# Kernel tuning notes

Hardware: AMD Instinct MI355X
Metric: run time of the kernel (lower is better)

## Reference

```python
import jax, jax.numpy as jnp
import numpy as np

B, S, D = 32, 1024, 1025  # batch, seq_length(=num_loci), input_dim
QD, KD = 64, 64
INIT_SCALE = 0.03


def _attention(y, Wq, Wk, Wv):
    # y: [B, S, D]
    q = jnp.einsum('bsd,dq->bsq', y, Wq)
    k = jnp.einsum('bsd,dk->bsk', y, Wk)
    v = jnp.einsum('bsd,de->bse', y, Wv)
    scores = jax.nn.softmax(jnp.einsum('bsq,btq->bst', q, k), axis=-1)
    return jnp.einsum('bst,bte->bse', scores, v)


def setup_inputs() -> dict:
    key = jax.random.key(0)
    ks = jax.random.split(key, 13)
    p = lambda k, shape: INIT_SCALE * jax.random.normal(k, shape, dtype=jnp.float32)
    return {
        'x': jax.random.normal(ks[0], (B, S, D), dtype=jnp.float32),
        'Wq1': p(ks[1], (D, QD)), 'Wk1': p(ks[2], (D, KD)), 'Wv1': p(ks[3], (D, D)),
        'Wq2': p(ks[4], (D, QD)), 'Wk2': p(ks[5], (D, KD)), 'Wv2': p(ks[6], (D, D)),
        'Wq3': p(ks[7], (D, QD)), 'Wk3': p(ks[8], (D, KD)), 'Wv3': p(ks[9], (D, D)),
        'random_matrix': p(ks[10], (S, D - 1)),
        'coeffs_attended': p(ks[11], (S, D)),
        'offset': p(ks[12], (1,)),
    }


def reference(x, Wq1, Wk1, Wv1, Wq2, Wk2, Wv2, Wq3, Wk3, Wv3,
              random_matrix, coeffs_attended, offset):
    # y = concat(x[:, :, :S] @ random_matrix, x[:, :, -1:])  -> [B, S, D]
    y = jnp.concatenate(
        [jnp.einsum('bsf,fe->bse', x[:, :, :S], random_matrix), x[:, :, -1:]],
        axis=2)
    a1 = _attention(y, Wq1, Wk1, Wv1)
    a2 = _attention(a1, Wq2, Wk2, Wv2)
    a3 = _attention(a2, Wq3, Wk3, Wv3)
    out = jnp.einsum('bij,ij->b', a3, coeffs_attended) + offset
    return out
```

## Files before the change

### kernel.cpp

```cpp
#include <hip/hip_runtime.h>
#include <hip/hip_bf16.h>
#include <stdint.h>

typedef __bf16 bf16;
typedef __bf16 bf16x8 __attribute__((ext_vector_type(8)));
typedef float f32x4 __attribute__((ext_vector_type(4)));
typedef float f32x8u __attribute__((ext_vector_type(8)));
typedef f32x8u f32x8a __attribute__((aligned(4)));

__device__ __forceinline__ void gl16(const void* g, void* lds) {
  __builtin_amdgcn_global_load_lds(
      (const __attribute__((address_space(1))) void*)g,
      (__attribute__((address_space(3))) void*)lds, 16, 0, 0);
}

template <int OUT>
__global__ __launch_bounds__(256) void gemm_hr(
    const bf16* __restrict__ Ah, const bf16* __restrict__ Ar, int lda,
    long long sA_, const bf16* __restrict__ Bh, const bf16* __restrict__ Br,
    int ldb, long long sB_, float* __restrict__ Cf, bf16* __restrict__ Ch,
    bf16* __restrict__ Cr, int ldc, long long sC_, int N, int K, int ntn) {
  __shared__ bf16 tAh[128][32], tAr[128][32], tBh[128][32], tBr[128][32];

  const int tid = threadIdx.x;
  const int lane = tid & 63, wave = tid >> 6;
  const int wm = wave & 1, wn = wave >> 1;
  const int fr = lane & 15, fq = lane >> 4;

  const long long bz = blockIdx.y;
  Ah += bz * sA_;
  Ar += bz * sA_;
  Bh += bz * sB_;
  Br += bz * sB_;

  const int cpx = gridDim.x >> 3;
  const int b2 = (blockIdx.x & 7) * cpx + (blockIdx.x >> 3);
  const int tm = b2 / ntn, tn = b2 % ntn;
  const int m0 = tm * 128, n0 = tn * 128;

  const int c0 = wave * 128 + lane;
  const int colsw = (((c0 & 3) ^ ((c0 >> 3) & 3)) << 3);
  const int rA0 = m0 + (c0 >> 2);
  int rB0 = n0 + (c0 >> 2), rB1 = rB0 + 16;
  rB0 = rB0 < N ? rB0 : N - 1;
  rB1 = rB1 < N ? rB1 : N - 1;
  const long long offA0 = (long long)rA0 * lda + colsw;
  const long long offA1 = offA0 + (long long)16 * lda;
  const long long offB0 = (long long)rB0 * ldb + colsw;
  const long long offB1 = (long long)rB1 * ldb + colsw;

  char* dAh = (char*)&tAh[0][0] + wave * 2048;
  char* dAr = (char*)&tAr[0][0] + wave * 2048;
  char* dBh = (char*)&tBh[0][0] + wave * 2048;
  char* dBr = (char*)&tBr[0][0] + wave * 2048;

  const int colA = ((fq ^ ((fr >> 1) & 3)) << 3);

  f32x4 acc[4][4] = {};
  const int nk = K >> 5;
  for (int kt = 0; kt < nk; ++kt) {
    const int k0 = kt << 5;
    gl16(Ah + offA0 + k0, dAh);
    gl16(Ah + offA1 + k0, dAh + 1024);
    gl16(Ar + offA0 + k0, dAr);
    gl16(Ar + offA1 + k0, dAr + 1024);
    gl16(Bh + offB0 + k0, dBh);
    gl16(Bh + offB1 + k0, dBh + 1024);
    gl16(Br + offB0 + k0, dBr);
    gl16(Br + offB1 + k0, dBr + 1024);
    __syncthreads();

    bf16x8 ah[4], ar_[4], bh[4], br_[4];
#pragma unroll
    for (int i = 0; i < 4; ++i) {
      ah[i] = *reinterpret_cast<const bf16x8*>(&tAh[wm * 64 + i * 16 + fr][colA]);
      ar_[i] = *reinterpret_cast<const bf16x8*>(&tAr[wm * 64 + i * 16 + fr][colA]);
      bh[i] = *reinterpret_cast<const bf16x8*>(&tBh[wn * 64 + i * 16 + fr][colA]);
      br_[i] = *reinterpret_cast<const bf16x8*>(&tBr[wn * 64 + i * 16 + fr][colA]);
    }
#pragma unroll
    for (int mi = 0; mi < 4; ++mi)
#pragma unroll
      for (int ni = 0; ni < 4; ++ni)
        acc[mi][ni] = __builtin_amdgcn_mfma_f32_16x16x32_bf16(
            ah[mi], bh[ni], acc[mi][ni], 0, 0, 0);
#pragma unroll
    for (int mi = 0; mi < 4; ++mi)
#pragma unroll
      for (int ni = 0; ni < 4; ++ni)
        acc[mi][ni] = __builtin_amdgcn_mfma_f32_16x16x32_bf16(
            ah[mi], br_[ni], acc[mi][ni], 0, 0, 0);
#pragma unroll
    for (int mi = 0; mi < 4; ++mi)
#pragma unroll
      for (int ni = 0; ni < 4; ++ni)
        acc[mi][ni] = __builtin_amdgcn_mfma_f32_16x16x32_bf16(
            ar_[mi], bh[ni], acc[mi][ni], 0, 0, 0);
    __syncthreads();
  }

  if constexpr (OUT == 0) {
    float* C = Cf + bz * sC_;
#pragma unroll
    for (int mi = 0; mi < 4; ++mi)
#pragma unroll
      for (int ni = 0; ni < 4; ++ni) {
        int cc = n0 + wn * 64 + ni * 16 + fr;
        if (cc < N) {
          long long base = (long long)(m0 + wm * 64 + mi * 16 + fq * 4) * ldc + cc;
#pragma unroll
          for (int j = 0; j < 4; ++j) C[base + (long long)j * ldc] = acc[mi][ni][j];
        }
      }
  } else {
    bf16* CH = Ch + bz * sC_;
    bf16* CR = Cr + bz * sC_;
#pragma unroll
    for (int mi = 0; mi < 4; ++mi)
#pragma unroll
      for (int ni = 0; ni < 4; ++ni) {
        int cc = n0 + wn * 64 + ni * 16 + fr;
        if (cc < N) {
          long long base = (long long)(m0 + wm * 64 + mi * 16 + fq * 4) * ldc + cc;
#pragma unroll
          for (int j = 0; j < 4; ++j) {
            float v = acc[mi][ni][j];
            bf16 h = (bf16)v;
            CH[base + (long long)j * ldc] = h;
            CR[base + (long long)j * ldc] = (bf16)(v - (float)h);
          }
        }
      }
  }
}

template <int OUT>
__global__ __launch_bounds__(256, 2) void gemm_hr2(
    const bf16* __restrict__ Ah, const bf16* __restrict__ Ar, int lda,
    long long sA_, const bf16* __restrict__ Bh, const bf16* __restrict__ Br,
    int ldb, long long sB_, float* __restrict__ Cf, bf16* __restrict__ Ch,
    bf16* __restrict__ Cr, int ldc, long long sC_, int N, int K, int ntn,
    const float* __restrict__ Rinv) {
  __shared__ bf16 tAh[256][32], tAr[256][32], tBh[128][32], tBr[128][32];

  const int tid = threadIdx.x;
  const int lane = tid & 63, wave = tid >> 6;
  const int wm = wave & 1, wn = wave >> 1;
  const int fr = lane & 15, fq = lane >> 4;

  const long long bz = blockIdx.y;
  Ah += bz * sA_;
  Ar += bz * sA_;
  Bh += bz * sB_;
  Br += bz * sB_;

  const int nwg = gridDim.x;
  const int q = nwg >> 3, r = nwg & 7;
  const int xcd = blockIdx.x & 7, o8 = blockIdx.x >> 3;
  const int b2 = (xcd < r ? xcd * (q + 1) : r * (q + 1) + (xcd - r) * q) + o8;
  const int tm = b2 / ntn, tn = b2 % ntn;
  const int m0 = tm * 256, n0 = tn * 128;

  const int cA = wave * 64 + lane;
  const int colsw = (((cA & 3) ^ ((cA >> 3) & 3)) << 3);
  const int rA = cA >> 2;
  const long long offA = (long long)(m0 + rA) * lda + colsw;
  const long long strA = (long long)64 * lda;
  int rB0 = n0 + rA, rB1 = n0 + rA + 64;
  rB0 = rB0 < N ? rB0 : N - 1;
  rB1 = rB1 < N ? rB1 : N - 1;
  const long long offB0 = (long long)rB0 * ldb + colsw;
  const long long offB1 = (long long)rB1 * ldb + colsw;

  char* dAh = (char*)&tAh[0][0] + wave * 1024;
  char* dAr = (char*)&tAr[0][0] + wave * 1024;
  char* dBh = (char*)&tBh[0][0] + wave * 1024;
  char* dBr = (char*)&tBr[0][0] + wave * 1024;

  const int colA = ((fq ^ ((fr >> 1) & 3)) << 3);

  f32x4 acc[8][4] = {};
  const int nk = K >> 5;
  for (int kt = 0; kt < nk; ++kt) {
    const int k0 = kt << 5;
#pragma unroll
    for (int j = 0; j < 4; ++j) {
      gl16(Ah + offA + j * strA + k0, dAh + j * 4096);
      gl16(Ar + offA + j * strA + k0, dAr + j * 4096);
    }
    gl16(Bh + offB0 + k0, dBh);
    gl16(Bh + offB1 + k0, dBh + 4096);
    gl16(Br + offB0 + k0, dBr);
    gl16(Br + offB1 + k0, dBr + 4096);
    __syncthreads();

    bf16x8 bh[4], br_[4];
#pragma unroll
    for (int i = 0; i < 4; ++i) {
      bh[i] = *reinterpret_cast<const bf16x8*>(&tBh[wn * 64 + i * 16 + fr][colA]);
      br_[i] = *reinterpret_cast<const bf16x8*>(&tBr[wn * 64 + i * 16 + fr][colA]);
    }
#pragma unroll
    for (int mi = 0; mi < 8; ++mi) {
      bf16x8 ah = *reinterpret_cast<const bf16x8*>(
          &tAh[wm * 128 + mi * 16 + fr][colA]);
      bf16x8 ar_ = *reinterpret_cast<const bf16x8*>(
          &tAr[wm * 128 + mi * 16 + fr][colA]);
#pragma unroll
      for (int ni = 0; ni < 4; ++ni)
        acc[mi][ni] = __builtin_amdgcn_mfma_f32_16x16x32_bf16(
            ah, bh[ni], acc[mi][ni], 0, 0, 0);
#pragma unroll
      for (int ni = 0; ni < 4; ++ni)
        acc[mi][ni] = __builtin_amdgcn_mfma_f32_16x16x32_bf16(
            ah, br_[ni], acc[mi][ni], 0, 0, 0);
#pragma unroll
      for (int ni = 0; ni < 4; ++ni)
        acc[mi][ni] = __builtin_amdgcn_mfma_f32_16x16x32_bf16(
            ar_, bh[ni], acc[mi][ni], 0, 0, 0);
    }
    __syncthreads();
  }

  if constexpr (OUT == 0) {
    float* C = Cf + bz * sC_;
#pragma unroll
    for (int mi = 0; mi < 8; ++mi)
#pragma unroll
      for (int ni = 0; ni < 4; ++ni) {
        int cc = n0 + wn * 64 + ni * 16 + fr;
        if (cc < N) {
          long long base =
              (long long)(m0 + wm * 128 + mi * 16 + fq * 4) * ldc + cc;
#pragma unroll
          for (int j = 0; j < 4; ++j) C[base + (long long)j * ldc] = acc[mi][ni][j];
        }
      }
  } else if constexpr (OUT == 1) {
    bf16* CH = Ch + bz * sC_;
    bf16* CR = Cr + bz * sC_;
    const float* rz = Rinv ? Rinv + bz * 1024 : nullptr;
#pragma unroll
    for (int mi = 0; mi < 8; ++mi)
#pragma unroll
      for (int ni = 0; ni < 4; ++ni) {
        int cc = n0 + wn * 64 + ni * 16 + fr;
        if (cc < N) {
          int gr = m0 + wm * 128 + mi * 16 + fq * 4;
          long long base = (long long)gr * ldc + cc;
#pragma unroll
          for (int j = 0; j < 4; ++j) {
            float v = acc[mi][ni][j];
            if (rz) v *= rz[gr + j];
            bf16 h = (bf16)v;
            CH[base + (long long)j * ldc] = h;
            CR[base + (long long)j * ldc] = (bf16)(v - (float)h);
          }
        }
      }
  } else if constexpr (OUT == 2) {
    bf16* CH = Ch + bz * sC_;
    bf16* CR = Cr + bz * sC_;
#pragma unroll
    for (int mi = 0; mi < 8; ++mi)
#pragma unroll
      for (int ni = 0; ni < 4; ++ni) {
        int cc = n0 + wn * 64 + ni * 16 + fr;
        if (cc < N) {
          int mr = m0 + wm * 128 + mi * 16 + fq * 4;
          union { bf16 h[4]; uint2 u; } th, tr;
#pragma unroll
          for (int j = 0; j < 4; ++j) {
            float v = acc[mi][ni][j];
            bf16 h = (bf16)v;
            th.h[j] = h;
            tr.h[j] = (bf16)(v - (float)h);
          }
          *reinterpret_cast<uint2*>(CH + (long long)cc * ldc + mr) = th.u;
          *reinterpret_cast<uint2*>(CR + (long long)cc * ldc + mr) = tr.u;
        }
      }
  } else {
    bf16* CH = Ch + bz * sC_;
    bf16* CR = Cr + bz * sC_;
#pragma unroll
    for (int mi = 0; mi < 8; ++mi)
#pragma unroll
      for (int ni = 0; ni < 4; ++ni) {
        int cc = n0 + wn * 64 + ni * 16 + fr;
        if (cc < N) {
          long long base =
              (long long)(m0 + wm * 128 + mi * 16 + fq * 4) * ldc + cc;
#pragma unroll
          for (int j = 0; j < 4; ++j) {
            float v = __expf(acc[mi][ni][j]);
            bf16 h = (bf16)v;
            CH[base + (long long)j * ldc] = h;
            CR[base + (long long)j * ldc] = (bf16)(v - (float)h);
          }
        }
      }
  }
}

__global__ __launch_bounds__(256, 2) void gemm_dot1(
    const bf16* __restrict__ Ah, int lda, long long sA_,
    const bf16* __restrict__ Bh, int ldb, long long sB_, int N, int K,
    int ntn, const float* __restrict__ G, int ldg,
    const float* __restrict__ Rinv, float* __restrict__ partial) {
  __shared__ bf16 tAh[256][32], tBh[128][32];

  const int tid = threadIdx.x;
  const int lane = tid & 63, wave = tid >> 6;
  const int wm = wave & 1, wn = wave >> 1;
  const int fr = lane & 15, fq = lane >> 4;

  const long long bz = blockIdx.y;
  Ah += bz * sA_;
  Bh += bz * sB_;
  const float* rz = Rinv + bz * 1024;

  const int nwg = gridDim.x;
  const int q = nwg >> 3, r = nwg & 7;
  const int xcd = blockIdx.x & 7, o8 = blockIdx.x >> 3;
  const int b2 = (xcd < r ? xcd * (q + 1) : r * (q + 1) + (xcd - r) * q) + o8;
  const int tm = b2 / ntn, tn = b2 % ntn;
  const int m0 = tm * 256, n0 = tn * 128;

  const int cA = wave * 64 + lane;
  const int colsw = (((cA & 3) ^ ((cA >> 3) & 3)) << 3);
  const int rA = cA >> 2;
  const long long offA = (long long)(m0 + rA) * lda + colsw;
  const long long strA = (long long)64 * lda;
  int rB0 = n0 + rA, rB1 = n0 + rA + 64;
  rB0 = rB0 < N ? rB0 : N - 1;
  rB1 = rB1 < N ? rB1 : N - 1;
  const long long offB0 = (long long)rB0 * ldb + colsw;
  const long long offB1 = (long long)rB1 * ldb + colsw;

  char* dAh = (char*)&tAh[0][0] + wave * 1024;
  char* dBh = (char*)&tBh[0][0] + wave * 1024;

  const int colA = ((fq ^ ((fr >> 1) & 3)) << 3);

  f32x4 acc[8][4] = {};
  const int nk = K >> 5;
  for (int kt = 0; kt < nk; ++kt) {
    const int k0 = kt << 5;
#pragma unroll
    for (int j = 0; j < 4; ++j) gl16(Ah + offA + j * strA + k0, dAh + j * 4096);
    gl16(Bh + offB0 + k0, dBh);
    gl16(Bh + offB1 + k0, dBh + 4096);
    __syncthreads();

    bf16x8 bh[4];
#pragma unroll
    for (int i = 0; i < 4; ++i)
      bh[i] = *reinterpret_cast<const bf16x8*>(&tBh[wn * 64 + i * 16 + fr][colA]);
#pragma unroll
    for (int mi = 0; mi < 8; ++mi) {
      bf16x8 ah = *reinterpret_cast<const bf16x8*>(
          &tAh[wm * 128 + mi * 16 + fr][colA]);
#pragma unroll
      for (int ni = 0; ni < 4; ++ni)
        acc[mi][ni] = __builtin_amdgcn_mfma_f32_16x16x32_bf16(
            ah, bh[ni], acc[mi][ni], 0, 0, 0);
    }
    __syncthreads();
  }

  float dot = 0.f;
#pragma unroll
  for (int mi = 0; mi < 8; ++mi)
#pragma unroll
    for (int ni = 0; ni < 4; ++ni) {
      int cc = n0 + wn * 64 + ni * 16 + fr;
      if (cc < N) {
        int gr = m0 + wm * 128 + mi * 16 + fq * 4;
        long long base = (long long)gr * ldg + cc;
#pragma unroll
        for (int j = 0; j < 4; ++j)
          dot += acc[mi][ni][j] * rz[gr + j] * G[base + (long long)j * ldg];
      }
    }
#pragma unroll
  for (int o = 32; o; o >>= 1) dot += __shfl_xor(dot, o);
  float* red = (float*)&tAh[0][0];
  if (lane == 0) red[wave] = dot;
  __syncthreads();
  if (tid == 0)
    partial[bz * gridDim.x + b2] = red[0] + red[1] + red[2] + red[3];
}

__global__ __launch_bounds__(256, 2) void gemm0w(
    const float* __restrict__ A, int lda, const float* __restrict__ B, int ldb,
    bf16* __restrict__ Ch, bf16* __restrict__ Cr, int ldc, int N, int K,
    int ntn) {
  __shared__ bf16 tAh[256][32], tAr[256][32], tBh[128][32], tBr[128][32];

  const int tid = threadIdx.x;
  const int lane = tid & 63, wave = tid >> 6;
  const int wm = wave & 1, wn = wave >> 1;
  const int fr = lane & 15, fq = lane >> 4;

  const int nwg = gridDim.x;
  const int q = nwg >> 3, r = nwg & 7;
  const int xcd = blockIdx.x & 7, o8 = blockIdx.x >> 3;
  const int b2 = (xcd < r ? xcd * (q + 1) : r * (q + 1) + (xcd - r) * q) + o8;
  const int tm = b2 / ntn, tn = b2 % ntn;
  const int m0 = tm * 256, n0 = tn * 128;

  const int row0 = tid >> 2, slot = tid & 3;
  const int wcol = ((slot ^ ((tid >> 3) & 3)) << 3);
  const int colA = ((fq ^ ((fr >> 1) & 3)) << 3);

  f32x4 acc[8][4] = {};
  const int nk = K >> 5;
  for (int kt = 0; kt < nk; ++kt) {
    const int k0 = kt << 5;
    f32x8a ra[4], rb[2];
#pragma unroll
    for (int p = 0; p < 4; ++p) {
      int row = row0 + p * 64;
      ra[p] = *reinterpret_cast<const f32x8a*>(
          A + (long long)(m0 + row) * lda + k0 + slot * 8);
    }
#pragma unroll
    for (int p = 0; p < 2; ++p) {
      int n = n0 + row0 + p * 64;
      n = n < N ? n : N - 1;
      rb[p] = *reinterpret_cast<const f32x8a*>(
          B + (long long)n * ldb + k0 + slot * 8);
    }
    __syncthreads();
#pragma unroll
    for (int p = 0; p < 4; ++p) {
      int row = row0 + p * 64;
      bf16x8 vh, vr;
#pragma unroll
      for (int j = 0; j < 8; ++j) {
        float f = ra[p][j];
        bf16 h = (bf16)f;
        vh[j] = h;
        vr[j] = (bf16)(f - (float)h);
      }
      *reinterpret_cast<bf16x8*>(&tAh[row][wcol]) = vh;
      *reinterpret_cast<bf16x8*>(&tAr[row][wcol]) = vr;
    }
#pragma unroll
    for (int p = 0; p < 2; ++p) {
      int row = row0 + p * 64;
      bf16x8 vh, vr;
#pragma unroll
      for (int j = 0; j < 8; ++j) {
        float f = rb[p][j];
        bf16 h = (bf16)f;
        vh[j] = h;
        vr[j] = (bf16)(f - (float)h);
      }
      *reinterpret_cast<bf16x8*>(&tBh[row][wcol]) = vh;
      *reinterpret_cast<bf16x8*>(&tBr[row][wcol]) = vr;
    }
    __syncthreads();

    bf16x8 bh[4], br_[4];
#pragma unroll
    for (int i = 0; i < 4; ++i) {
      bh[i] = *reinterpret_cast<const bf16x8*>(&tBh[wn * 64 + i * 16 + fr][colA]);
      br_[i] = *reinterpret_cast<const bf16x8*>(&tBr[wn * 64 + i * 16 + fr][colA]);
    }
#pragma unroll
    for (int mi = 0; mi < 8; ++mi) {
      bf16x8 ah = *reinterpret_cast<const bf16x8*>(
          &tAh[wm * 128 + mi * 16 + fr][colA]);
      bf16x8 ar_ = *reinterpret_cast<const bf16x8*>(
          &tAr[wm * 128 + mi * 16 + fr][colA]);
#pragma unroll
      for (int ni = 0; ni < 4; ++ni)
        acc[mi][ni] = __builtin_amdgcn_mfma_f32_16x16x32_bf16(
            ah, bh[ni], acc[mi][ni], 0, 0, 0);
#pragma unroll
      for (int ni = 0; ni < 4; ++ni)
        acc[mi][ni] = __builtin_amdgcn_mfma_f32_16x16x32_bf16(
            ah, br_[ni], acc[mi][ni], 0, 0, 0);
#pragma unroll
      for (int ni = 0; ni < 4; ++ni)
        acc[mi][ni] = __builtin_amdgcn_mfma_f32_16x16x32_bf16(
            ar_, bh[ni], acc[mi][ni], 0, 0, 0);
    }
  }

#pragma unroll
  for (int mi = 0; mi < 8; ++mi)
#pragma unroll
    for (int ni = 0; ni < 4; ++ni) {
      int cc = n0 + wn * 64 + ni * 16 + fr;
      if (cc < N) {
        long long base =
            (long long)(m0 + wm * 128 + mi * 16 + fq * 4) * ldc + cc;
#pragma unroll
        for (int j = 0; j < 4; ++j) {
          float v = acc[mi][ni][j];
          bf16 h = (bf16)v;
          Ch[base + (long long)j * ldc] = h;
          Cr[base + (long long)j * ldc] = (bf16)(v - (float)h);
        }
      }
    }
}

template <int SPLIT>
__global__ __launch_bounds__(256) void transpose_tile(
    const float* __restrict__ src, int R, int Cc, float* __restrict__ df,
    bf16* __restrict__ dh, bf16* __restrict__ dr, int Nout, int outC,
    int ntk) {
  __shared__ float t[32][33];
  const int nt = blockIdx.x / ntk, kt = blockIdx.x % ntk;
  const int n0 = nt * 32, k0 = kt * 32;
  const int c = threadIdx.x & 31, r0 = threadIdx.x >> 5;
#pragma unroll
  for (int p = 0; p < 4; ++p) {
    int k = k0 + r0 + p * 8, n = n0 + c;
    t[r0 + p * 8][c] = (k < R && n < Cc) ? src[(long long)k * Cc + n] : 0.f;
  }
  __syncthreads();
#pragma unroll
  for (int p = 0; p < 4; ++p) {
    int n = n0 + r0 + p * 8, k = k0 + c;
    if (n < Nout && k < outC) {
      float v = t[c][r0 + p * 8];
      long long idx = (long long)n * outC + k;
      if constexpr (SPLIT) {
        bf16 h = (bf16)v;
        dh[idx] = h;
        dr[idx] = (bf16)(v - (float)h);
      } else {
        df[idx] = v;
      }
    }
  }
}

__global__ __launch_bounds__(256) void transpose_h(
    const ushort* __restrict__ sh, ushort* __restrict__ dh) {
  __shared__ ushort lh[32][33];
  const long long b = blockIdx.y;
  const int et = blockIdx.x >> 5, tt = blockIdx.x & 31;
  const int e0 = et * 32, t0 = tt * 32;
  const int c = threadIdx.x & 31, r0 = threadIdx.x >> 5;
  const ushort* sh_b = sh + b * 1024 * 1056;
#pragma unroll
  for (int p = 0; p < 4; ++p) {
    int t = t0 + r0 + p * 8;
    lh[r0 + p * 8][c] = sh_b[(long long)t * 1056 + e0 + c];
  }
  __syncthreads();
  ushort* dh_b = dh + b * 1056 * 1024;
#pragma unroll
  for (int p = 0; p < 4; ++p) {
    int e = e0 + r0 + p * 8;
    dh_b[(long long)e * 1024 + t0 + c] = lh[c][r0 + p * 8];
  }
}

__global__ __launch_bounds__(256) void pad_split_g(
    const float* __restrict__ src, int R, int Cc, bf16* __restrict__ dh,
    bf16* __restrict__ dr, long long total, int outC) {
  long long idx = (long long)blockIdx.x * 256 + threadIdx.x;
  if (idx >= total) return;
  int n = (int)(idx / outC), k = (int)(idx % outC);
  float v = (n < R && k < Cc) ? src[(long long)n * Cc + k] : 0.f;
  bf16 h = (bf16)v;
  dh[idx] = h;
  dr[idx] = (bf16)(v - (float)h);
}

__global__ __launch_bounds__(256) void fixup_y_split(bf16* __restrict__ Yh,
                                                     bf16* __restrict__ Yr,
                                                     const float* __restrict__ x) {
  int row = blockIdx.x * 256 + threadIdx.x;
  if (row < 32768) {
    float v = x[(long long)row * 1025 + 1024];
    bf16 h = (bf16)v;
    long long base = (long long)row * 1056;
    Yh[base + 1024] = h;
    Yr[base + 1024] = (bf16)(v - (float)h);
#pragma unroll
    for (int c = 1025; c < 1056; ++c) {
      Yh[base + c] = (bf16)0.f;
      Yr[base + c] = (bf16)0.f;
    }
  }
}

__global__ __launch_bounds__(256) void rowsum_k(const bf16* __restrict__ Eh,
                                                const bf16* __restrict__ Er,
                                                float* __restrict__ rinv) {
  long long row = blockIdx.x;
  const bf16* ph = Eh + row * 1024;
  const bf16* pr = Er + row * 1024;
  int tid = threadIdx.x;
  float s = 0.f;
#pragma unroll
  for (int j = 0; j < 4; ++j)
    s += (float)ph[tid + 256 * j] + (float)pr[tid + 256 * j];
#pragma unroll
  for (int o = 32; o; o >>= 1) s += __shfl_xor(s, o);
  __shared__ float ss[4];
  if ((tid & 63) == 0) ss[tid >> 6] = s;
  __syncthreads();
  if (tid == 0) rinv[row] = 1.0f / (ss[0] + ss[1] + ss[2] + ss[3]);
}

__global__ void finalize_k(const float* __restrict__ partial,
                           const float* __restrict__ offs,
                           float* __restrict__ out, int per_b) {
  int b = threadIdx.x;
  if (b < 32) {
    float s = 0.f;
    for (int i = 0; i < per_b; ++i) s += partial[b * per_b + i];
    out[b] = s + offs[0];
  }
}


extern "C" void kernel_launch(void* const* d_in, const int* in_sizes, int n_in,
                              void* d_out, int out_size, void* d_ws,
                              size_t ws_size, hipStream_t stream) {
  const float* x = (const float*)d_in[0];
  const float* Wq[3] = {(const float*)d_in[1], (const float*)d_in[4],
                        (const float*)d_in[7]};
  const float* Wk[3] = {(const float*)d_in[2], (const float*)d_in[5],
                        (const float*)d_in[8]};
  const float* Wv[3] = {(const float*)d_in[3], (const float*)d_in[6],
                        (const float*)d_in[9]};
  const float* R = (const float*)d_in[10];
  const float* coef = (const float*)d_in[11];
  const float* offs = (const float*)d_in[12];
  float* out = (float*)d_out;

  const int CB = (ws_size >= (size_t)340000000ULL) ? 16 : 8;
  const int NCH = 32 / CB;

  char* ws = (char*)d_ws;
  size_t off = 0;
  auto alloc = [&](size_t bytes) -> void* {
    void* p = ws + off;
    off = (off + bytes + 255) & ~(size_t)255;
    return p;
  };
  bf16* Yh = (bf16*)alloc(32768LL * 1056 * 2);
  bf16* Yr = (bf16*)alloc(32768LL * 1056 * 2);
  bf16* qkh = (bf16*)alloc(32768LL * 128 * 2);
  bf16* qkr = (bf16*)alloc(32768LL * 128 * 2);
  bf16* Ph = (bf16*)alloc((long long)CB * 1024 * 1024 * 2);
  bf16* Pr = (bf16*)alloc((long long)CB * 1024 * 1024 * 2);
  bf16* vTh = (bf16*)alloc((long long)CB * 1056 * 1024 * 2);
  bf16* vTr = (bf16*)alloc((long long)CB * 1056 * 1024 * 2);
  float* rinv = (float*)alloc((long long)CB * 1024 * 4);
  float* RT = (float*)alloc(1024LL * 1024 * 4);
  bf16 *WqkTh[3], *WqkTr[3], *WvTh[3], *WvTr[3];
  for (int i = 0; i < 3; ++i) {
    WqkTh[i] = (bf16*)alloc(128LL * 1056 * 2);
    WqkTr[i] = (bf16*)alloc(128LL * 1056 * 2);
    WvTh[i] = (bf16*)alloc(1056LL * 1056 * 2);
    WvTr[i] = (bf16*)alloc(1056LL * 1056 * 2);
  }
  bf16* coefh = (bf16*)alloc(1024LL * 1056 * 2);
  bf16* coefr = (bf16*)alloc(1024LL * 1056 * 2);
  float* G = (float*)alloc(1024LL * 1056 * 4);
  float* partial = (float*)alloc(32 * 36 * 4);

  transpose_tile<0><<<32 * 32, 256, 0, stream>>>(R, 1024, 1024, RT, nullptr,
                                                 nullptr, 1024, 1024, 32);
  for (int l = 0; l < 3; ++l) {
    transpose_tile<1><<<33 * 2, 256, 0, stream>>>(
        Wq[l], 1025, 64, nullptr, WqkTh[l], WqkTr[l], 64, 1056, 33);
    transpose_tile<1><<<33 * 2, 256, 0, stream>>>(
        Wk[l], 1025, 64, nullptr, WqkTh[l] + 64 * 1056, WqkTr[l] + 64 * 1056,
        64, 1056, 33);
    if (l < 2) {
      transpose_tile<1><<<33 * 33, 256, 0, stream>>>(
          Wv[l], 1025, 1025, nullptr, WvTh[l], WvTr[l], 1056, 1056, 33);
    } else {
      pad_split_g<<<4356, 256, 0, stream>>>(Wv[l], 1025, 1025, WvTh[l],
                                            WvTr[l], 1056LL * 1056, 1056);
    }
  }
  pad_split_g<<<4224, 256, 0, stream>>>(coef, 1024, 1025, coefh, coefr,
                                        1024LL * 1056, 1056);
  gemm_hr<0><<<dim3(72, 1), 256, 0, stream>>>(
      coefh, coefr, 1056, 0, WvTh[2], WvTr[2], 1056, 0, G, nullptr, nullptr,
      1056, 0, 1056, 1056, 9);

  gemm0w<<<dim3(1024, 1), 256, 0, stream>>>(x, 1025, RT, 1024, Yh, Yr, 1056,
                                            1024, 1024, 8);
  fixup_y_split<<<128, 256, 0, stream>>>(Yh, Yr, x);

  for (int l = 0; l < 3; ++l) {
    gemm_hr<1><<<dim3(256, 1), 256, 0, stream>>>(
        Yh, Yr, 1056, 0, WqkTh[l], WqkTr[l], 1056, 0, nullptr, qkh, qkr, 128,
        0, 128, 1056, 1);
    for (int ch = 0; ch < NCH; ++ch) {
      const long long b0 = (long long)ch * CB;
      bf16* Ych = Yh + b0 * 1024 * 1056;
      bf16* Ycr = Yr + b0 * 1024 * 1056;
      bf16* qkch = qkh + b0 * 1024 * 128;
      bf16* qkcr = qkr + b0 * 1024 * 128;
      if (l < 2) {
        gemm_hr2<2><<<dim3(36, CB), 256, 0, stream>>>(
            Ych, Ycr, 1056, 1024LL * 1056, WvTh[l], WvTr[l], 1056, 0, nullptr,
            vTh, vTr, 1024, 1056LL * 1024, 1056, 1056, 9, nullptr);
      } else {
        transpose_h<<<dim3(33 * 32, CB), 256, 0, stream>>>(
            (const ushort*)Ych, (ushort*)vTh);
      }
      gemm_hr2<4><<<dim3(32, CB), 256, 0, stream>>>(
          qkch, qkcr, 128, 1024LL * 128, qkch + 64, qkcr + 64, 128,
          1024LL * 128, nullptr, Ph, Pr, 1024, 1024LL * 1024, 1024, 64, 8,
          nullptr);
      rowsum_k<<<CB * 1024, 256, 0, stream>>>(Ph, Pr, rinv);
      if (l < 2) {
        gemm_hr2<1><<<dim3(36, CB), 256, 0, stream>>>(
            Ph, Pr, 1024, 1024LL * 1024, vTh, vTr, 1024, 1056LL * 1024,
            nullptr, Ych, Ycr, 1056, 1024LL * 1056, 1056, 1024, 9, rinv);
      } else {
        gemm_dot1<<<dim3(36, CB), 256, 0, stream>>>(
            Ph, 1024, 1024LL * 1024, vTh, 1024, 1056LL * 1024, 1056, 1024, 9,
            G, 1056, rinv, partial + b0 * 36);
      }
    }
  }

  finalize_k<<<1, 32, 0, stream>>>(partial, offs, out, 36);
}
```

Baseline: 2.341 ms.

## Replace fused exp-split score epilogue with fp32 logits and stable softmax kernel

The QK^T GEMM now writes fp32 logits instead of exponentiating and splitting them into bf16 hi/lo in its epilogue. A new per-row kernel does a max-subtracted softmax, normalizes, and writes the bf16 hi/lo probabilities, skipping the residual for the last layer. The downstream GEMMs drop the per-row reciprocal scaling. This makes the softmax numerically stable, but it adds an fp32 logits buffer and an extra write and read of it per chunk, and it raises the workspace threshold for the large chunk size.

```diff
diff --git a/kernel.cpp b/kernel.cpp
--- a/kernel.cpp
+++ b/kernel.cpp
@@ -139,8 +139,7 @@
     const bf16* __restrict__ Ah, const bf16* __restrict__ Ar, int lda,
     long long sA_, const bf16* __restrict__ Bh, const bf16* __restrict__ Br,
     int ldb, long long sB_, float* __restrict__ Cf, bf16* __restrict__ Ch,
-    bf16* __restrict__ Cr, int ldc, long long sC_, int N, int K, int ntn,
-    const float* __restrict__ Rinv) {
+    bf16* __restrict__ Cr, int ldc, long long sC_, int N, int K, int ntn) {
   __shared__ bf16 tAh[256][32], tAr[256][32], tBh[128][32], tBr[128][32];
 
   const int tid = threadIdx.x;
@@ -239,26 +238,24 @@
   } else if constexpr (OUT == 1) {
     bf16* CH = Ch + bz * sC_;
     bf16* CR = Cr + bz * sC_;
-    const float* rz = Rinv ? Rinv + bz * 1024 : nullptr;
 #pragma unroll
     for (int mi = 0; mi < 8; ++mi)
 #pragma unroll
       for (int ni = 0; ni < 4; ++ni) {
         int cc = n0 + wn * 64 + ni * 16 + fr;
         if (cc < N) {
-          int gr = m0 + wm * 128 + mi * 16 + fq * 4;
-          long long base = (long long)gr * ldc + cc;
+          long long base =
+              (long long)(m0 + wm * 128 + mi * 16 + fq * 4) * ldc + cc;
 #pragma unroll
           for (int j = 0; j < 4; ++j) {
             float v = acc[mi][ni][j];
-            if (rz) v *= rz[gr + j];
             bf16 h = (bf16)v;
             CH[base + (long long)j * ldc] = h;
             CR[base + (long long)j * ldc] = (bf16)(v - (float)h);
           }
         }
       }
-  } else if constexpr (OUT == 2) {
+  } else {
     bf16* CH = Ch + bz * sC_;
     bf16* CR = Cr + bz * sC_;
 #pragma unroll
@@ -280,26 +277,6 @@
           *reinterpret_cast<uint2*>(CR + (long long)cc * ldc + mr) = tr.u;
         }
       }
-  } else {
-    bf16* CH = Ch + bz * sC_;
-    bf16* CR = Cr + bz * sC_;
-#pragma unroll
-    for (int mi = 0; mi < 8; ++mi)
-#pragma unroll
-      for (int ni = 0; ni < 4; ++ni) {
-        int cc = n0 + wn * 64 + ni * 16 + fr;
-        if (cc < N) {
-          long long base =
-              (long long)(m0 + wm * 128 + mi * 16 + fq * 4) * ldc + cc;
-#pragma unroll
-          for (int j = 0; j < 4; ++j) {
-            float v = __expf(acc[mi][ni][j]);
-            bf16 h = (bf16)v;
-            CH[base + (long long)j * ldc] = h;
-            CR[base + (long long)j * ldc] = (bf16)(v - (float)h);
-          }
-        }
-      }
   }
 }
 
@@ -307,7 +284,7 @@
     const bf16* __restrict__ Ah, int lda, long long sA_,
     const bf16* __restrict__ Bh, int ldb, long long sB_, int N, int K,
     int ntn, const float* __restrict__ G, int ldg,
-    const float* __restrict__ Rinv, float* __restrict__ partial) {
+    float* __restrict__ partial) {
   __shared__ bf16 tAh[256][32], tBh[128][32];
 
   const int tid = threadIdx.x;
@@ -318,7 +295,6 @@
   const long long bz = blockIdx.y;
   Ah += bz * sA_;
   Bh += bz * sB_;
-  const float* rz = Rinv + bz * 1024;
 
   const int nwg = gridDim.x;
   const int q = nwg >> 3, r = nwg & 7;
@@ -376,11 +352,11 @@
     for (int ni = 0; ni < 4; ++ni) {
       int cc = n0 + wn * 64 + ni * 16 + fr;
       if (cc < N) {
-        int gr = m0 + wm * 128 + mi * 16 + fq * 4;
-        long long base = (long long)gr * ldg + cc;
+        long long base =
+            (long long)(m0 + wm * 128 + mi * 16 + fq * 4) * ldg + cc;
 #pragma unroll
         for (int j = 0; j < 4; ++j)
-          dot += acc[mi][ni][j] * rz[gr + j] * G[base + (long long)j * ldg];
+          dot += acc[mi][ni][j] * G[base + (long long)j * ldg];
       }
     }
 #pragma unroll
@@ -593,23 +569,42 @@
   }
 }
 
-__global__ __launch_bounds__(256) void rowsum_k(const bf16* __restrict__ Eh,
-                                                const bf16* __restrict__ Er,
-                                                float* __restrict__ rinv) {
+__global__ __launch_bounds__(256) void softmax_split(
+    const float* __restrict__ Plog, bf16* __restrict__ Ph,
+    bf16* __restrict__ Pr, int wr) {
   long long row = blockIdx.x;
-  const bf16* ph = Eh + row * 1024;
-  const bf16* pr = Er + row * 1024;
+  const float* p = Plog + row * 1024;
   int tid = threadIdx.x;
+  float v[4];
+#pragma unroll
+  for (int j = 0; j < 4; ++j) v[j] = p[tid + 256 * j];
+  float m = fmaxf(fmaxf(v[0], v[1]), fmaxf(v[2], v[3]));
+#pragma unroll
+  for (int o = 32; o; o >>= 1) m = fmaxf(m, __shfl_xor(m, o));
+  __shared__ float sm[4];
+  if ((tid & 63) == 0) sm[tid >> 6] = m;
+  __syncthreads();
+  m = fmaxf(fmaxf(sm[0], sm[1]), fmaxf(sm[2], sm[3]));
   float s = 0.f;
 #pragma unroll
-  for (int j = 0; j < 4; ++j)
-    s += (float)ph[tid + 256 * j] + (float)pr[tid + 256 * j];
+  for (int j = 0; j < 4; ++j) {
+    v[j] = __expf(v[j] - m);
+    s += v[j];
+  }
 #pragma unroll
   for (int o = 32; o; o >>= 1) s += __shfl_xor(s, o);
   __shared__ float ss[4];
   if ((tid & 63) == 0) ss[tid >> 6] = s;
   __syncthreads();
-  if (tid == 0) rinv[row] = 1.0f / (ss[0] + ss[1] + ss[2] + ss[3]);
+  s = ss[0] + ss[1] + ss[2] + ss[3];
+  float inv = 1.0f / s;
+#pragma unroll
+  for (int j = 0; j < 4; ++j) {
+    float pv = v[j] * inv;
+    bf16 h = (bf16)pv;
+    Ph[row * 1024 + tid + 256 * j] = h;
+    if (wr) Pr[row * 1024 + tid + 256 * j] = (bf16)(pv - (float)h);
+  }
 }
 
 __global__ void finalize_k(const float* __restrict__ partial,
@@ -639,7 +634,7 @@
   const float* offs = (const float*)d_in[12];
   float* out = (float*)d_out;
 
-  const int CB = (ws_size >= (size_t)340000000ULL) ? 16 : 8;
+  const int CB = (ws_size >= (size_t)390000000ULL) ? 16 : 8;
   const int NCH = 32 / CB;
 
   char* ws = (char*)d_ws;
@@ -653,11 +648,11 @@
   bf16* Yr = (bf16*)alloc(32768LL * 1056 * 2);
   bf16* qkh = (bf16*)alloc(32768LL * 128 * 2);
   bf16* qkr = (bf16*)alloc(32768LL * 128 * 2);
+  float* Plog = (float*)alloc((long long)CB * 1024 * 1024 * 4);
   bf16* Ph = (bf16*)alloc((long long)CB * 1024 * 1024 * 2);
   bf16* Pr = (bf16*)alloc((long long)CB * 1024 * 1024 * 2);
   bf16* vTh = (bf16*)alloc((long long)CB * 1056 * 1024 * 2);
   bf16* vTr = (bf16*)alloc((long long)CB * 1056 * 1024 * 2);
-  float* rinv = (float*)alloc((long long)CB * 1024 * 4);
   float* RT = (float*)alloc(1024LL * 1024 * 4);
   bf16 *WqkTh[3], *WqkTr[3], *WvTh[3], *WvTr[3];
   for (int i = 0; i < 3; ++i) {
@@ -710,24 +705,24 @@
       if (l < 2) {
         gemm_hr2<2><<<dim3(36, CB), 256, 0, stream>>>(
             Ych, Ycr, 1056, 1024LL * 1056, WvTh[l], WvTr[l], 1056, 0, nullptr,
-            vTh, vTr, 1024, 1056LL * 1024, 1056, 1056, 9, nullptr);
+            vTh, vTr, 1024, 1056LL * 1024, 1056, 1056, 9);
       } else {
         transpose_h<<<dim3(33 * 32, CB), 256, 0, stream>>>(
             (const ushort*)Ych, (ushort*)vTh);
       }
-      gemm_hr2<4><<<dim3(32, CB), 256, 0, stream>>>(
+      gemm_hr2<0><<<dim3(32, CB), 256, 0, stream>>>(
           qkch, qkcr, 128, 1024LL * 128, qkch + 64, qkcr + 64, 128,
-          1024LL * 128, nullptr, Ph, Pr, 1024, 1024LL * 1024, 1024, 64, 8,
-          nullptr);
-      rowsum_k<<<CB * 1024, 256, 0, stream>>>(Ph, Pr, rinv);
+          1024LL * 128, Plog, nullptr, nullptr, 1024, 1024LL * 1024, 1024, 64,
+          8);
+      softmax_split<<<CB * 1024, 256, 0, stream>>>(Plog, Ph, Pr, l < 2 ? 1 : 0);
       if (l < 2) {
         gemm_hr2<1><<<dim3(36, CB), 256, 0, stream>>>(
             Ph, Pr, 1024, 1024LL * 1024, vTh, vTr, 1024, 1056LL * 1024,
-            nullptr, Ych, Ycr, 1056, 1024LL * 1056, 1056, 1024, 9, rinv);
+            nullptr, Ych, Ycr, 1056, 1024LL * 1056, 1056, 1024, 9);
       } else {
         gemm_dot1<<<dim3(36, CB), 256, 0, stream>>>(
             Ph, 1024, 1024LL * 1024, vTh, 1024, 1056LL * 1024, 1056, 1024, 9,
-            G, 1056, rinv, partial + b0 * 36);
+            G, 1056, partial + b0 * 36);
       }
     }
   }
```

After: 2.280 ms. 1.03x faster.
